# Performance work log

Hardware: AMD Instinct MI355X
Metric: run time of the kernel (lower is better)

The kernel has to match this reference:

```python
import jax, jax.numpy as jnp
import numpy as np

EPS = 1e-5
BS, NA, NC, NL, NPTS, ED, NG = 1, 900, 6, 4, 13, 256, 8
GD = ED // NG
IMG_W, IMG_H = 704.0, 256.0
FMAP_HW = [(64, 176), (32, 88), (16, 44), (8, 22)]


def _ln(x, g, b):
    m = x.mean(-1, keepdims=True)
    v = ((x - m) ** 2).mean(-1, keepdims=True)
    return (x - m) / jnp.sqrt(v + EPS) * g + b


def _grid_sample(img, grid):
    # img: [N,C,H,W]; grid: [N,P,Q,2] in [-1,1]; bilinear, zeros padding, align_corners=False
    N, C, H, W = img.shape
    gx = jnp.clip((grid[..., 0] + 1.0) * (W * 0.5) - 0.5, -1e4, 1e4)
    gy = jnp.clip((grid[..., 1] + 1.0) * (H * 0.5) - 0.5, -1e4, 1e4)
    x0 = jnp.floor(gx); y0 = jnp.floor(gy)
    wx1 = gx - x0; wy1 = gy - y0; wx0 = 1.0 - wx1; wy0 = 1.0 - wy1
    x0i = x0.astype(jnp.int32); y0i = y0.astype(jnp.int32)
    flat = img.reshape(N, C, H * W)

    def corner(xi, yi, wgt):
        valid = (xi >= 0) & (xi < W) & (yi >= 0) & (yi < H)
        idx = (jnp.clip(yi, 0, H - 1) * W + jnp.clip(xi, 0, W - 1))
        g = jax.vmap(lambda f, i: f[:, i])(flat, idx.reshape(N, -1))  # [N,C,P*Q]
        g = g.reshape(N, C, idx.shape[1], idx.shape[2])
        return g * (wgt * valid)[:, None]

    return (corner(x0i, y0i, wx0 * wy0) + corner(x0i + 1, y0i, wx1 * wy0)
            + corner(x0i, y0i + 1, wx0 * wy1) + corner(x0i + 1, y0i + 1, wx1 * wy1))


def setup_inputs() -> dict:
    key = jax.random.key(0)
    ks = jax.random.split(key, 20)
    d = {}
    d['instance_feature'] = jax.random.normal(ks[0], (BS, NA, ED), jnp.float32)
    xyz = jax.random.normal(ks[1], (BS, NA, 3), jnp.float32) * 1.5
    size = jax.random.normal(ks[2], (BS, NA, 3), jnp.float32) * 0.3
    theta = jax.random.uniform(ks[3], (BS, NA, 1), jnp.float32) * (2.0 * np.pi)
    vel = jax.random.normal(ks[4], (BS, NA, 3), jnp.float32) * 0.1
    d['anchor'] = jnp.concatenate([xyz, size, jnp.sin(theta), jnp.cos(theta), vel], -1)
    d['anchor_embed'] = jax.random.normal(ks[5], (BS, NA, ED), jnp.float32)
    for i, (h, w) in enumerate(FMAP_HW):
        d[f'fmap{i}'] = jax.random.normal(ks[6 + i], (BS, NC, ED, h, w), jnp.float32)
    base = jnp.array([[80., 0., 0., 352.], [0., 80., 0., 128.],
                      [0., 0., 0., 1.], [0., 0., 0., 1.]], jnp.float32)
    proj = jnp.tile(base, (BS, NC, 1, 1))
    proj = proj.at[:, :, :2, :].add(jax.random.normal(ks[10], (BS, NC, 2, 4), jnp.float32) * 2.0)
    d['projection_mat'] = proj
    d['image_wh'] = jnp.broadcast_to(jnp.array([IMG_W, IMG_H], jnp.float32), (BS, NC, 2))
    d['fix_scale'] = jnp.array([[0, 0, 0], [0.45, 0, 0], [-0.45, 0, 0], [0, 0.45, 0],
                                [0, -0.45, 0], [0, 0, 0.45], [0, 0, -0.45]], jnp.float32)

    def w(k, shape):
        return jax.random.normal(k, shape, jnp.float32) * 0.02

    d['lfc_w'] = w(ks[11], (ED, 6 * 3)); d['lfc_b'] = jnp.zeros((18,), jnp.float32)
    d['cam_w1'] = w(ks[12], (12, ED)); d['cam_b1'] = jnp.zeros((ED,), jnp.float32)
    d['cam_g1'] = jnp.ones((ED,), jnp.float32); d['cam_be1'] = jnp.zeros((ED,), jnp.float32)
    d['cam_w2'] = w(ks[13], (ED, ED)); d['cam_b2'] = jnp.zeros((ED,), jnp.float32)
    d['cam_g2'] = jnp.ones((ED,), jnp.float32); d['cam_be2'] = jnp.zeros((ED,), jnp.float32)
    d['wfc_w'] = w(ks[14], (ED, NG * NL * NPTS)); d['wfc_b'] = jnp.zeros((NG * NL * NPTS,), jnp.float32)
    d['op_w'] = w(ks[15], (ED, ED)); d['op_b'] = jnp.zeros((ED,), jnp.float32)
    return d


def reference(instance_feature, anchor, anchor_embed, fmap0, fmap1, fmap2, fmap3,
              projection_mat, image_wh, fix_scale, lfc_w, lfc_b,
              cam_w1, cam_b1, cam_g1, cam_be1, cam_w2, cam_b2, cam_g2, cam_be2,
              wfc_w, wfc_b, op_w, op_b):
    bs, na = instance_feature.shape[:2]
    # ---- keypoint generation ----
    size = jnp.exp(anchor[..., None, 3:6])                       # [bs,na,1,3]
    kp = fix_scale * size                                        # [bs,na,7,3]
    ls = jax.nn.sigmoid(instance_feature @ lfc_w + lfc_b).reshape(bs, na, -1, 3) - 0.5
    kp = jnp.concatenate([kp, ls * size], axis=-2)               # [bs,na,NPTS,3]
    sin, cos = anchor[..., 6:7], anchor[..., 7:8]                # [bs,na,1]
    kx, ky, kz = kp[..., 0], kp[..., 1], kp[..., 2]
    key_points = jnp.stack([cos * kx - sin * ky, sin * kx + cos * ky, kz], -1) \
                 + anchor[..., None, 0:3]                        # [bs,na,NPTS,3]
    # ---- per-cam/level/point group weights ----
    feat = instance_feature + anchor_embed
    cam_in = projection_mat[:, :, :3].reshape(bs, NC, 12)
    h = jax.nn.relu(cam_in @ cam_w1 + cam_b1); h = _ln(h, cam_g1, cam_be1)
    h = jax.nn.relu(h @ cam_w2 + cam_b2); cam_embed = _ln(h, cam_g2, cam_be2)
    f = feat[:, :, None] + cam_embed[:, None]                    # [bs,na,NC,ED]
    wts = (f @ wfc_w + wfc_b).reshape(bs, na, NC * NL * NPTS, NG)
    wts = jax.nn.softmax(wts, axis=-2).reshape(bs, na, NC, NL, NPTS, NG)
    # ---- multi-cam projection + bilinear sampling ----
    pts = jnp.concatenate([key_points, jnp.ones_like(key_points[..., :1])], -1)
    p2d = jnp.einsum('bcij,banj->bcani', projection_mat, pts)    # [bs,NC,na,NPTS,4]
    p2d = p2d[..., :2] / jnp.maximum(p2d[..., 2:3], 1e-5)
    p2d = p2d / image_wh[:, :, None, None]
    grid = (p2d * 2.0 - 1.0).reshape(bs * NC, na, NPTS, 2)
    feats = jnp.stack([_grid_sample(fm.reshape(bs * NC, ED, fm.shape[-2], fm.shape[-1]), grid)
                       for fm in (fmap0, fmap1, fmap2, fmap3)], axis=1)  # [bs*NC,NL,ED,na,NPTS]
    feats = feats.reshape(bs, NC, NL, ED, na, NPTS).transpose(0, 4, 1, 2, 5, 3)  # [bs,na,NC,NL,NPTS,ED]
    # ---- group-weighted fusion over cams & levels, then sum over points ----
    fg = feats.reshape(bs, na, NC, NL, NPTS, NG, GD)
    fused = jnp.einsum('bnclpg,bnclpgd->bnpgd', wts, fg).reshape(bs, na, NPTS, ED)
    fused = fused.sum(axis=2)                                    # [bs,na,ED]
    out = fused @ op_w + op_b
    return jnp.concatenate([out, instance_feature], axis=-1)     # [bs,na,2*ED]
```

## Files before the change

kernel.cpp:

```cpp
#include <hip/hip_runtime.h>
#include <stdint.h>

#define NA 900
#define NC 6
#define NL 4
#define NPTS 13
#define ED 256
#define NG 8
#define LNEPS 1e-5f
#define NSTAGE 718303
#define NSTAGE_BLOCKS 2806
#define NTRANS 1416
#define NCOPY 672
#define NSAMP 312
#define LGS 313

struct PIn { const void* p[24]; };

__device__ __forceinline__ float b2f(unsigned short u){
  union { uint32_t i; float f; } v; v.i = ((uint32_t)u)<<16; return v.f;
}
__device__ __forceinline__ unsigned short f2b(float f){
  union { float f; uint32_t i; } v; v.f = f;
  uint32_t r = v.i + 0x7FFFu + ((v.i>>16)&1u);
  return (unsigned short)(r>>16);
}
#define BLO(u) __uint_as_float((u)<<16)
#define BHI(u) __uint_as_float((u)&0xffff0000u)

__device__ __forceinline__ float ldx(const void* p, int i, bool bf){
  return bf ? b2f(((const unsigned short*)p)[i]) : ((const float*)p)[i];
}

__device__ __forceinline__ bool sniff_bf(const unsigned short* __restrict__ u16){
  int lane = threadIdx.x & 63;
  unsigned short u = u16[2*lane];
  int e = (u>>7)&0xFF;
  int sane = (e>=110 && e<=135) ? 1 : 0;
  #pragma unroll
  for (int m=32;m;m>>=1) sane += __shfl_xor(sane, m);
  return sane >= 48;
}

__device__ __forceinline__ void blockReduce2(float& a, float& b, float* lds){
  #pragma unroll
  for (int m=32;m;m>>=1){ a += __shfl_xor(a,m); b += __shfl_xor(b,m); }
  int w = threadIdx.x>>6;
  if ((threadIdx.x&63)==0){ lds[w]=a; lds[w+4]=b; }
  __syncthreads();
  a = lds[0]+lds[1]+lds[2]+lds[3];
  b = lds[4]+lds[5]+lds[6]+lds[7];
  __syncthreads();
}

__global__ __launch_bounds__(256) void k_prep(PIn in, float* __restrict__ stage,
                                              unsigned short* __restrict__ tf,
                                              unsigned short* __restrict__ wfcw_h,
                                              unsigned short* __restrict__ opw_h,
                                              float* __restrict__ Bc){
  const bool bf = sniff_bf((const unsigned short*)in.p[0]);
  const int tid = threadIdx.x;
  int b = blockIdx.x;

  __shared__ unsigned short TT[64][64];
  __shared__ float h[ED];
  __shared__ float cE[ED];
  __shared__ float red8[8];
  __shared__ float part[4][64];

  if (b < NSTAGE_BLOCKS){
    const int cum[21] = {0,230400,240300,470700,470796,470808,470829,475437,475455,
                         478527,478783,479039,479295,544831,545087,545343,545599,
                         652095,652511,718047,718303};
    const int map[20] = {0,1,2,7,8,9,10,11,12,13,14,15,16,17,18,19,20,21,22,23};
    int idx = b*256 + tid;
    if (idx >= NSTAGE) return;
    int seg = 0, base = 0;
    #pragma unroll
    for (int s=1;s<20;s++) if (idx >= cum[s]){ seg = s; base = cum[s]; }
    const void* src = in.p[map[0]];
    #pragma unroll
    for (int s=1;s<20;s++) if (seg==s) src = in.p[map[s]];
    stage[idx] = ldx(src, idx - base, bf);
    return;
  }
  b -= NSTAGE_BLOCKS;
  if (b < NTRANS){
    const int tiles[4] = {44,11,3,1};
    const int HWs[4]   = {11264,2816,704,176};
    const int TFO[4]   = {0,17301504,21626880,22708224};
    int l, local;
    if      (b < 1056){ l=0; local=b;      }
    else if (b < 1320){ l=1; local=b-1056; }
    else if (b < 1392){ l=2; local=b-1320; }
    else              { l=3; local=b-1392; }
    int pt = local % tiles[l]; int rest = local / tiles[l];
    int ct = rest & 3; int c = rest >> 2;
    const int HW = HWs[l];
    const int px0 = pt*256;
    const void* src = in.p[3+l];
    const int j8 = tid & 7;
    const int w8 = tid >> 3;

    uint4 v[2][4];
    if (bf){
      #pragma unroll
      for (int p=0;p<2;p++){
        int ch = ct*64 + p*32 + w8;
        size_t rowb = (size_t)(c*ED+ch)*HW;
        #pragma unroll
        for (int q=0;q<4;q++){
          int pxs = px0 + q*64 + j8*8;
          if (pxs < HW)
            v[p][q] = *reinterpret_cast<const uint4*>((const unsigned short*)src + rowb + pxs);
          else
            v[p][q] = make_uint4(0,0,0,0);
        }
      }
    }
    for (int q=0;q<4;q++){
      if (px0 + q*64 >= HW) break;
      if (!bf){
        #pragma unroll
        for (int p=0;p<2;p++){
          int ch = ct*64 + p*32 + w8;
          size_t rowb = (size_t)(c*ED+ch)*HW;
          int pxs = px0 + q*64 + j8*8;
          if (pxs < HW){
            float4 f0 = *reinterpret_cast<const float4*>((const float*)src + rowb + pxs);
            float4 f1 = *reinterpret_cast<const float4*>((const float*)src + rowb + pxs + 4);
            v[p][q].x = (uint32_t)f2b(f0.x) | ((uint32_t)f2b(f0.y)<<16);
            v[p][q].y = (uint32_t)f2b(f0.z) | ((uint32_t)f2b(f0.w)<<16);
            v[p][q].z = (uint32_t)f2b(f1.x) | ((uint32_t)f2b(f1.y)<<16);
            v[p][q].w = (uint32_t)f2b(f1.z) | ((uint32_t)f2b(f1.w)<<16);
          } else v[p][q] = make_uint4(0,0,0,0);
        }
      }
      #pragma unroll
      for (int p=0;p<2;p++){
        int r = p*32 + w8;
        int g8 = (j8 ^ (r>>3))<<3;
        *reinterpret_cast<uint4*>(&TT[r][g8]) = v[p][q];
      }
      __syncthreads();
      #pragma unroll
      for (int p=0;p<2;p++){
        int pxl = p*32 + w8;
        int px  = px0 + q*64 + pxl;
        int colq = (((pxl>>3) ^ j8)<<3) | (pxl & 7);
        int rb = j8*8;
        unsigned short t0 = TT[rb+0][colq], t1 = TT[rb+1][colq];
        unsigned short t2 = TT[rb+2][colq], t3 = TT[rb+3][colq];
        unsigned short t4 = TT[rb+4][colq], t5 = TT[rb+5][colq];
        unsigned short t6 = TT[rb+6][colq], t7 = TT[rb+7][colq];
        uint4 o;
        o.x = (uint32_t)t0 | ((uint32_t)t1<<16);
        o.y = (uint32_t)t2 | ((uint32_t)t3<<16);
        o.z = (uint32_t)t4 | ((uint32_t)t5<<16);
        o.w = (uint32_t)t6 | ((uint32_t)t7<<16);
        if (px < HW)
          *reinterpret_cast<uint4*>(tf + TFO[l] + (size_t)c*HW*ED + (size_t)px*ED + ct*64 + j8*8) = o;
      }
      __syncthreads();
    }
    return;
  }
  b -= NTRANS;
  if (b < NCOPY){
    int idx = b*256 + tid;
    if (idx < 106496){
      wfcw_h[idx] = bf ? ((const unsigned short*)in.p[20])[idx]
                       : f2b(((const float*)in.p[20])[idx]);
    } else {
      int j = idx - 106496;
      opw_h[j] = bf ? ((const unsigned short*)in.p[22])[j]
                    : f2b(((const float*)in.p[22])[j]);
    }
    return;
  }
  b -= NCOPY;
  {
    const void* proj = in.p[7];
    const void* w1 = in.p[12]; const void* b1 = in.p[13];
    const void* g1 = in.p[14]; const void* be1 = in.p[15];
    const void* w2 = in.p[16]; const void* b2 = in.p[17];
    const void* g2 = in.p[18]; const void* be2 = in.p[19];
    const void* wfcw = in.p[20]; const void* wfcb = in.p[21];
    const int c = b/7, colt = b - (b/7)*7;
    float ci[12];
    #pragma unroll
    for (int i=0;i<12;i++) ci[i] = ldx(proj, c*16+i, bf);
    float acc = ldx(b1, tid, bf);
    #pragma unroll
    for (int k=0;k<12;k++) acc += ci[k]*ldx(w1, k*ED+tid, bf);
    float x = fmaxf(acc, 0.f);
    float s=x, q=x*x;
    blockReduce2(s,q,red8);
    float mean = s*(1.f/ED), var = q*(1.f/ED)-mean*mean;
    h[tid] = (x-mean)*rsqrtf(var+LNEPS)*ldx(g1,tid,bf) + ldx(be1,tid,bf);
    __syncthreads();
    acc = ldx(b2, tid, bf);
    #pragma unroll 8
    for (int k=0;k<ED;k++) acc += h[k]*ldx(w2, k*ED+tid, bf);
    x = fmaxf(acc,0.f);
    s=x; q=x*x;
    blockReduce2(s,q,red8);
    mean = s*(1.f/ED); var = q*(1.f/ED)-mean*mean;
    cE[tid] = (x-mean)*rsqrtf(var+LNEPS)*ldx(g2,tid,bf) + ldx(be2,tid,bf);
    __syncthreads();
    const int kc = tid>>6, colL = tid&63, col = colt*64+colL;
    float a = 0.f;
    if (col < 416){
      #pragma unroll 8
      for (int k=0;k<64;k++) a += cE[kc*64+k]*ldx(wfcw, (kc*64+k)*416+col, bf);
    }
    part[kc][colL] = a;
    __syncthreads();
    if (kc==0 && col<416)
      Bc[c*416+col] = part[0][colL]+part[1][colL]+part[2][colL]+part[3][colL] + ldx(wfcb,col,bf);
  }
}

__global__ __launch_bounds__(512, 4) void k_anchor(
    const float* __restrict__ stage, const unsigned short* __restrict__ tf,
    const unsigned short* __restrict__ wfcw_h, const unsigned short* __restrict__ opw_h,
    const float* __restrict__ Bc, const void* __restrict__ rawinst,
    void* __restrict__ outv){
  const int n = blockIdx.x, tid = threadIdx.x;
  const bool bf = sniff_bf((const unsigned short*)rawinst);

  const float* s_inst = stage + 0;
  const float* s_anc  = stage + 230400;
  const float* s_ae   = stage + 240300;
  const float* s_proj = stage + 470700;
  const float* s_imwh = stage + 470796;
  const float* s_fixs = stage + 470808;
  const float* s_lw   = stage + 470829;
  const float* s_lb   = stage + 475437;
  const float* s_opb  = stage + 718047;

  __shared__ float ifs[ED];
  __shared__ float fe[ED];
  __shared__ float lg2[8*LGS];
  __shared__ uint4 cbi[NSAMP];
  __shared__ uint4 cwf[NSAMP];
  __shared__ unsigned short coff[NSAMP];
  __shared__ float red[16][ED+4];
  __shared__ float fu[ED];
  __shared__ float kp[13][3];
  __shared__ float sc[8];
  __shared__ float lsv[18];
  __shared__ int scnt;

  if (tid < 256){
    float iv = s_inst[n*ED+tid];
    ifs[tid] = iv;
    fe[tid]  = iv + s_ae[n*ED+tid];
  } else {
    int t = tid - 256;
    if (t == 0)      scnt = 0;
    if (t < 3)       sc[t] = s_anc[n*11+t];
    else if (t == 3) sc[3] = s_anc[n*11+6];
    else if (t == 4) sc[4] = s_anc[n*11+7];
    else if (t < 8)  sc[t] = __expf(s_anc[n*11+t-2]);
  }
  __syncthreads();
  if (tid < 144){
    int d = tid>>3, j = tid&7;
    float a = 0.f;
    #pragma unroll 8
    for (int k=j*32;k<j*32+32;k++) a += ifs[k]*s_lw[k*18+d];
    a += __shfl_xor(a,1); a += __shfl_xor(a,2); a += __shfl_xor(a,4);
    if (j==0){
      a += s_lb[d];
      lsv[d] = 1.f/(1.f+__expf(-a)) - 0.5f;
    }
  }
  __syncthreads();
  if (tid < 13){
    float kx,ky,kz;
    if (tid < 7){
      kx = s_fixs[tid*3+0]*sc[5];
      ky = s_fixs[tid*3+1]*sc[6];
      kz = s_fixs[tid*3+2]*sc[7];
    } else {
      int j = tid-7;
      kx = lsv[j*3+0]*sc[5]; ky = lsv[j*3+1]*sc[6]; kz = lsv[j*3+2]*sc[7];
    }
    kp[tid][0] = sc[4]*kx - sc[3]*ky + sc[0];
    kp[tid][1] = sc[3]*kx + sc[4]*ky + sc[1];
    kp[tid][2] = kz + sc[2];
  }
  if (tid < 416){
    float a0 = 0.f;
    #pragma unroll 8
    for (int k=0;k<ED;k++) a0 += fe[k]*b2f(wfcw_h[k*416+tid]);
    const int g = tid & 7, rr = tid >> 3;
    #pragma unroll
    for (int c=0;c<NC;c++)
      lg2[g*LGS + c*52 + rr] = a0 + Bc[c*416+tid];
  }
  __syncthreads();
  if (tid < NSAMP){
    int s = tid;
    int c = s/52, rr = s - c*52;
    int l = rr/13, p = rr - l*13;
    float m[12];
    #pragma unroll
    for (int i=0;i<12;i++) m[i] = s_proj[c*16+i];
    float X=kp[p][0], Y=kp[p][1], Z=kp[p][2];
    float x = m[0]*X + m[1]*Y + m[2]*Z  + m[3];
    float y = m[4]*X + m[5]*Y + m[6]*Z  + m[7];
    float z = m[8]*X + m[9]*Y + m[10]*Z + m[11];
    float d = fmaxf(z, 1e-5f);
    float px = x/(d*s_imwh[c*2+0]), py = y/(d*s_imwh[c*2+1]);
    const int W = 176>>l, H = 64>>l;
    const int TFO[4] = {0,17301504,21626880,22708224};
    float gx = fminf(fmaxf(px*(float)W - 0.5f, -10000.f), 10000.f);
    float gy = fminf(fmaxf(py*(float)H - 0.5f, -10000.f), 10000.f);
    float xf = floorf(gx), yf = floorf(gy);
    int x0 = (int)xf, y0 = (int)yf;
    float wx1 = gx-xf, wy1 = gy-yf;
    float wx0 = 1.f-wx1, wy0 = 1.f-wy1;
    bool vx0 = (x0>=0)&&(x0<W),   vx1 = (x0+1>=0)&&(x0+1<W);
    bool vy0 = (y0>=0)&&(y0<H),   vy1 = (y0+1>=0)&&(y0+1<H);
    float w00 = (vx0&&vy0) ? wx0*wy0 : 0.f;
    float w10 = (vx1&&vy0) ? wx1*wy0 : 0.f;
    float w01 = (vx0&&vy1) ? wx0*wy1 : 0.f;
    float w11 = (vx1&&vy1) ? wx1*wy1 : 0.f;
    if (w00+w10+w01+w11 != 0.f){
      int cx0 = min(max(x0,0),W-1), cx1 = min(max(x0+1,0),W-1);
      int cy0 = min(max(y0,0),H-1), cy1 = min(max(y0+1,0),H-1);
      uint32_t cam = (uint32_t)TFO[l] + (uint32_t)(c*H*W)*ED;
      uint4 bi, wv;
      bi.x = cam + (uint32_t)(cy0*W+cx0)*ED;
      bi.y = cam + (uint32_t)(cy0*W+cx1)*ED;
      bi.z = cam + (uint32_t)(cy1*W+cx0)*ED;
      bi.w = cam + (uint32_t)(cy1*W+cx1)*ED;
      wv.x = __float_as_uint(w00); wv.y = __float_as_uint(w10);
      wv.z = __float_as_uint(w01); wv.w = __float_as_uint(w11);
      int slot = atomicAdd(&scnt, 1);
      cbi[slot] = bi;
      cwf[slot] = wv;
      coff[slot] = (unsigned short)s;
    }
  }
  {
    const int g = tid>>6, j = tid&63;
    float v[5]; float mx = -1e30f;
    #pragma unroll
    for (int i=0;i<5;i++){
      int e = j + 64*i;
      float val = -1e30f;
      if (e < NSAMP){
        val = lg2[g*LGS + e];
        mx = fmaxf(mx, val);
      }
      v[i] = val;
    }
    #pragma unroll
    for (int mk=32;mk;mk>>=1) mx = fmaxf(mx, __shfl_xor(mx, mk));
    float sum = 0.f;
    #pragma unroll
    for (int i=0;i<5;i++){
      if (j + 64*i < NSAMP){ float ex = __expf(v[i]-mx); v[i] = ex; sum += ex; }
    }
    #pragma unroll
    for (int mk=32;mk;mk>>=1) sum += __shfl_xor(sum, mk);
    float inv = 1.f/sum;
    #pragma unroll
    for (int i=0;i<5;i++){
      int e = j + 64*i;
      if (e < NSAMP) lg2[g*LGS + e] = v[i]*inv;
    }
  }
  __syncthreads();
  {
    const int m = scnt;
    const int strm = tid>>5, lane32 = tid&31;
    const int ch8 = lane32*8, gg = lane32>>2;
    float acc[8] = {0,0,0,0,0,0,0,0};
    int i = strm;
    for (; i + 16 < m; i += 32){
      uint4 biA = cbi[i],    wfA = cwf[i];
      uint4 biB = cbi[i+16], wfB = cwf[i+16];
      float wgA = lg2[gg*LGS + coff[i]],  wgB = lg2[gg*LGS + coff[i+16]];
      uint4 a00 = *reinterpret_cast<const uint4*>(tf + biA.x + ch8);
      uint4 a10 = *reinterpret_cast<const uint4*>(tf + biA.y + ch8);
      uint4 a01 = *reinterpret_cast<const uint4*>(tf + biA.z + ch8);
      uint4 a11 = *reinterpret_cast<const uint4*>(tf + biA.w + ch8);
      uint4 b00 = *reinterpret_cast<const uint4*>(tf + biB.x + ch8);
      uint4 b10 = *reinterpret_cast<const uint4*>(tf + biB.y + ch8);
      uint4 b01 = *reinterpret_cast<const uint4*>(tf + biB.z + ch8);
      uint4 b11 = *reinterpret_cast<const uint4*>(tf + biB.w + ch8);
      float pA00 = wgA*__uint_as_float(wfA.x), pA10 = wgA*__uint_as_float(wfA.y);
      float pA01 = wgA*__uint_as_float(wfA.z), pA11 = wgA*__uint_as_float(wfA.w);
      float pB00 = wgB*__uint_as_float(wfB.x), pB10 = wgB*__uint_as_float(wfB.y);
      float pB01 = wgB*__uint_as_float(wfB.z), pB11 = wgB*__uint_as_float(wfB.w);
      acc[0] += pA00*BLO(a00.x)+pA10*BLO(a10.x)+pA01*BLO(a01.x)+pA11*BLO(a11.x)
              + pB00*BLO(b00.x)+pB10*BLO(b10.x)+pB01*BLO(b01.x)+pB11*BLO(b11.x);
      acc[1] += pA00*BHI(a00.x)+pA10*BHI(a10.x)+pA01*BHI(a01.x)+pA11*BHI(a11.x)
              + pB00*BHI(b00.x)+pB10*BHI(b10.x)+pB01*BHI(b01.x)+pB11*BHI(b11.x);
      acc[2] += pA00*BLO(a00.y)+pA10*BLO(a10.y)+pA01*BLO(a01.y)+pA11*BLO(a11.y)
              + pB00*BLO(b00.y)+pB10*BLO(b10.y)+pB01*BLO(b01.y)+pB11*BLO(b11.y);
      acc[3] += pA00*BHI(a00.y)+pA10*BHI(a10.y)+pA01*BHI(a01.y)+pA11*BHI(a11.y)
              + pB00*BHI(b00.y)+pB10*BHI(b10.y)+pB01*BHI(b01.y)+pB11*BHI(b11.y);
      acc[4] += pA00*BLO(a00.z)+pA10*BLO(a10.z)+pA01*BLO(a01.z)+pA11*BLO(a11.z)
              + pB00*BLO(b00.z)+pB10*BLO(b10.z)+pB01*BLO(b01.z)+pB11*BLO(b11.z);
      acc[5] += pA00*BHI(a00.z)+pA10*BHI(a10.z)+pA01*BHI(a01.z)+pA11*BHI(a11.z)
              + pB00*BHI(b00.z)+pB10*BHI(b10.z)+pB01*BHI(b01.z)+pB11*BHI(b11.z);
      acc[6] += pA00*BLO(a00.w)+pA10*BLO(a10.w)+pA01*BLO(a01.w)+pA11*BLO(a11.w)
              + pB00*BLO(b00.w)+pB10*BLO(b10.w)+pB01*BLO(b01.w)+pB11*BLO(b11.w);
      acc[7] += pA00*BHI(a00.w)+pA10*BHI(a10.w)+pA01*BHI(a01.w)+pA11*BHI(a11.w)
              + pB00*BHI(b00.w)+pB10*BHI(b10.w)+pB01*BHI(b01.w)+pB11*BHI(b11.w);
    }
    for (; i < m; i += 16){
      uint4 bi = cbi[i], wf = cwf[i];
      float wg = lg2[gg*LGS + coff[i]];
      uint4 q00 = *reinterpret_cast<const uint4*>(tf + bi.x + ch8);
      uint4 q10 = *reinterpret_cast<const uint4*>(tf + bi.y + ch8);
      uint4 q01 = *reinterpret_cast<const uint4*>(tf + bi.z + ch8);
      uint4 q11 = *reinterpret_cast<const uint4*>(tf + bi.w + ch8);
      float p00 = wg*__uint_as_float(wf.x), p10 = wg*__uint_as_float(wf.y);
      float p01 = wg*__uint_as_float(wf.z), p11 = wg*__uint_as_float(wf.w);
      acc[0] += p00*BLO(q00.x)+p10*BLO(q10.x)+p01*BLO(q01.x)+p11*BLO(q11.x);
      acc[1] += p00*BHI(q00.x)+p10*BHI(q10.x)+p01*BHI(q01.x)+p11*BHI(q11.x);
      acc[2] += p00*BLO(q00.y)+p10*BLO(q10.y)+p01*BLO(q01.y)+p11*BLO(q11.y);
      acc[3] += p00*BHI(q00.y)+p10*BHI(q10.y)+p01*BHI(q01.y)+p11*BHI(q11.y);
      acc[4] += p00*BLO(q00.z)+p10*BLO(q10.z)+p01*BLO(q01.z)+p11*BLO(q11.z);
      acc[5] += p00*BHI(q00.z)+p10*BHI(q10.z)+p01*BHI(q01.z)+p11*BHI(q11.z);
      acc[6] += p00*BLO(q00.w)+p10*BLO(q10.w)+p01*BLO(q01.w)+p11*BLO(q11.w);
      acc[7] += p00*BHI(q00.w)+p10*BHI(q10.w)+p01*BHI(q01.w)+p11*BHI(q11.w);
    }
    *reinterpret_cast<float4*>(&red[strm][ch8])   = make_float4(acc[0],acc[1],acc[2],acc[3]);
    *reinterpret_cast<float4*>(&red[strm][ch8+4]) = make_float4(acc[4],acc[5],acc[6],acc[7]);
  }
  __syncthreads();
  if (tid < 256){
    float r = 0.f;
    #pragma unroll
    for (int i=0;i<16;i++) r += red[i][tid];
    fu[tid] = r;
  }
  __syncthreads();
  {
    const int col = tid & 255, half = tid >> 8;
    const int k0 = half*128;
    float a = 0.f;
    #pragma unroll 8
    for (int k=k0;k<k0+128;k++) a += fu[k]*b2f(opw_h[k*ED+col]);
    red[half][col] = a;
  }
  __syncthreads();
  {
    float v;
    if (tid < 256) v = s_opb[tid] + red[0][tid] + red[1][tid];
    else           v = ifs[tid-256];
    if (bf) ((unsigned short*)outv)[n*512+tid] = f2b(v);
    else    ((float*)outv)[n*512+tid]          = v;
  }
}

extern "C" void kernel_launch(void* const* d_in, const int* in_sizes, int n_in,
                              void* d_out, int out_size, void* d_ws, size_t ws_size,
                              hipStream_t stream){
  char* ws = (char*)d_ws;
  size_t off = 0;
  auto alloc = [&](size_t bytes)->char*{
    char* p = ws + off; off += (bytes + 63) & ~size_t(63); return p;
  };
  unsigned short* tf = (unsigned short*)alloc((size_t)22978560*2);
  float* stage  = (float*)alloc((size_t)NSTAGE*4);
  unsigned short* wfcw_h = (unsigned short*)alloc((size_t)106496*2);
  unsigned short* opw_h  = (unsigned short*)alloc((size_t)65536*2);
  float* Bc     = (float*)alloc((size_t)NC*416*4);

  PIn in;
  for (int i=0;i<24;i++) in.p[i] = d_in[i];

  k_prep<<<NSTAGE_BLOCKS + NTRANS + NCOPY + 42, 256, 0, stream>>>(in, stage, tf, wfcw_h, opw_h, Bc);
  k_anchor<<<NA, 512, 0, stream>>>(stage, tf, wfcw_h, opw_h, Bc, d_in[0], d_out);
}
```

Baseline: 253.9 us.

## Split anchor kernel into descriptor, split-gather and output-projection kernels

The single per-anchor kernel is replaced by three kernels. One builds the sampling descriptors, with softmax weights baked in, into global memory. One runs the bilinear gather with 4 blocks per anchor for more parallelism and occupancy. One reduces the partials and applies the output projection. This spreads the memory-bound gather over more blocks, at the cost of two extra launches and global round-trips for the descriptors and partial sums.

```diff
diff --git a/kernel.cpp b/kernel.cpp
--- a/kernel.cpp
+++ b/kernel.cpp
@@ -14,6 +14,8 @@
 #define NCOPY 672
 #define NSAMP 312
 #define LGS 313
+#define SPLITS 4
+#define CHMAX 78
 
 struct PIn { const void* p[24]; };
 
@@ -221,11 +223,10 @@
   }
 }
 
-__global__ __launch_bounds__(512, 4) void k_anchor(
-    const float* __restrict__ stage, const unsigned short* __restrict__ tf,
-    const unsigned short* __restrict__ wfcw_h, const unsigned short* __restrict__ opw_h,
+__global__ __launch_bounds__(256) void k_desc(
+    const float* __restrict__ stage, const unsigned short* __restrict__ wfcw_h,
     const float* __restrict__ Bc, const void* __restrict__ rawinst,
-    void* __restrict__ outv){
+    uint4* __restrict__ gdesc, int* __restrict__ mcnt, void* __restrict__ outv){
   const int n = blockIdx.x, tid = threadIdx.x;
   const bool bf = sniff_bf((const unsigned short*)rawinst);
 
@@ -237,32 +238,29 @@
   const float* s_fixs = stage + 470808;
   const float* s_lw   = stage + 470829;
   const float* s_lb   = stage + 475437;
-  const float* s_opb  = stage + 718047;
 
   __shared__ float ifs[ED];
   __shared__ float fe[ED];
   __shared__ float lg2[8*LGS];
-  __shared__ uint4 cbi[NSAMP];
-  __shared__ uint4 cwf[NSAMP];
-  __shared__ unsigned short coff[NSAMP];
-  __shared__ float red[16][ED+4];
-  __shared__ float fu[ED];
   __shared__ float kp[13][3];
   __shared__ float sc[8];
   __shared__ float lsv[18];
   __shared__ int scnt;
 
-  if (tid < 256){
+  {
+    if (tid==0) scnt = 0;
     float iv = s_inst[n*ED+tid];
     ifs[tid] = iv;
     fe[tid]  = iv + s_ae[n*ED+tid];
-  } else {
-    int t = tid - 256;
-    if (t == 0)      scnt = 0;
-    if (t < 3)       sc[t] = s_anc[n*11+t];
-    else if (t == 3) sc[3] = s_anc[n*11+6];
-    else if (t == 4) sc[4] = s_anc[n*11+7];
-    else if (t < 8)  sc[t] = __expf(s_anc[n*11+t-2]);
+    if (bf) ((unsigned short*)outv)[n*512+256+tid] = f2b(iv);
+    else    ((float*)outv)[n*512+256+tid]          = iv;
+    if (tid >= 256-8){
+      int t = tid - (256-8);
+      if (t < 3)       sc[t] = s_anc[n*11+t];
+      else if (t == 3) sc[3] = s_anc[n*11+6];
+      else if (t == 4) sc[4] = s_anc[n*11+7];
+      else             sc[t] = __expf(s_anc[n*11+t-2]);
+    }
   }
   __syncthreads();
   if (tid < 144){
@@ -291,174 +289,214 @@
     kp[tid][1] = sc[3]*kx + sc[4]*ky + sc[1];
     kp[tid][2] = kz + sc[2];
   }
-  if (tid < 416){
-    float a0 = 0.f;
-    #pragma unroll 8
-    for (int k=0;k<ED;k++) a0 += fe[k]*b2f(wfcw_h[k*416+tid]);
+  {
+    int col2 = (tid < 160) ? tid+256 : 415;
+    float a0 = 0.f, a1 = 0.f;
+    #pragma unroll 4
+    for (int k=0;k<ED;k++){
+      float fv = fe[k];
+      a0 += fv*b2f(wfcw_h[k*416+tid]);
+      a1 += fv*b2f(wfcw_h[k*416+col2]);
+    }
     const int g = tid & 7, rr = tid >> 3;
-    #pragma unroll
-    for (int c=0;c<NC;c++)
+    const int g2 = col2 & 7, rr2 = col2 >> 3;
+    #pragma unroll
+    for (int c=0;c<NC;c++){
       lg2[g*LGS + c*52 + rr] = a0 + Bc[c*416+tid];
-  }
-  __syncthreads();
-  if (tid < NSAMP){
-    int s = tid;
-    int c = s/52, rr = s - c*52;
-    int l = rr/13, p = rr - l*13;
-    float m[12];
-    #pragma unroll
-    for (int i=0;i<12;i++) m[i] = s_proj[c*16+i];
-    float X=kp[p][0], Y=kp[p][1], Z=kp[p][2];
-    float x = m[0]*X + m[1]*Y + m[2]*Z  + m[3];
-    float y = m[4]*X + m[5]*Y + m[6]*Z  + m[7];
-    float z = m[8]*X + m[9]*Y + m[10]*Z + m[11];
-    float d = fmaxf(z, 1e-5f);
-    float px = x/(d*s_imwh[c*2+0]), py = y/(d*s_imwh[c*2+1]);
-    const int W = 176>>l, H = 64>>l;
-    const int TFO[4] = {0,17301504,21626880,22708224};
-    float gx = fminf(fmaxf(px*(float)W - 0.5f, -10000.f), 10000.f);
-    float gy = fminf(fmaxf(py*(float)H - 0.5f, -10000.f), 10000.f);
-    float xf = floorf(gx), yf = floorf(gy);
-    int x0 = (int)xf, y0 = (int)yf;
-    float wx1 = gx-xf, wy1 = gy-yf;
-    float wx0 = 1.f-wx1, wy0 = 1.f-wy1;
-    bool vx0 = (x0>=0)&&(x0<W),   vx1 = (x0+1>=0)&&(x0+1<W);
-    bool vy0 = (y0>=0)&&(y0<H),   vy1 = (y0+1>=0)&&(y0+1<H);
-    float w00 = (vx0&&vy0) ? wx0*wy0 : 0.f;
-    float w10 = (vx1&&vy0) ? wx1*wy0 : 0.f;
-    float w01 = (vx0&&vy1) ? wx0*wy1 : 0.f;
-    float w11 = (vx1&&vy1) ? wx1*wy1 : 0.f;
-    if (w00+w10+w01+w11 != 0.f){
-      int cx0 = min(max(x0,0),W-1), cx1 = min(max(x0+1,0),W-1);
-      int cy0 = min(max(y0,0),H-1), cy1 = min(max(y0+1,0),H-1);
-      uint32_t cam = (uint32_t)TFO[l] + (uint32_t)(c*H*W)*ED;
-      uint4 bi, wv;
-      bi.x = cam + (uint32_t)(cy0*W+cx0)*ED;
-      bi.y = cam + (uint32_t)(cy0*W+cx1)*ED;
-      bi.z = cam + (uint32_t)(cy1*W+cx0)*ED;
-      bi.w = cam + (uint32_t)(cy1*W+cx1)*ED;
-      wv.x = __float_as_uint(w00); wv.y = __float_as_uint(w10);
-      wv.z = __float_as_uint(w01); wv.w = __float_as_uint(w11);
-      int slot = atomicAdd(&scnt, 1);
-      cbi[slot] = bi;
-      cwf[slot] = wv;
-      coff[slot] = (unsigned short)s;
-    }
-  }
+      if (tid < 160) lg2[g2*LGS + c*52 + rr2] = a1 + Bc[c*416+col2];
+    }
+  }
+  __syncthreads();
   {
-    const int g = tid>>6, j = tid&63;
-    float v[5]; float mx = -1e30f;
-    #pragma unroll
-    for (int i=0;i<5;i++){
-      int e = j + 64*i;
+    const int g = tid>>5, j = tid&31;
+    float v[10]; float mx = -1e30f;
+    #pragma unroll
+    for (int i=0;i<10;i++){
+      int e = j + 32*i;
       float val = -1e30f;
-      if (e < NSAMP){
-        val = lg2[g*LGS + e];
-        mx = fmaxf(mx, val);
+      if (e < NSAMP){ val = lg2[g*LGS + e]; mx = fmaxf(mx, val); }
+      v[i] = val;
+    }
+    #pragma unroll
+    for (int mk=16;mk;mk>>=1) mx = fmaxf(mx, __shfl_xor(mx, mk, 32));
+    float sum = 0.f;
+    #pragma unroll
+    for (int i=0;i<10;i++){
+      if (j + 32*i < NSAMP){ float ex = __expf(v[i]-mx); v[i] = ex; sum += ex; }
+    }
+    #pragma unroll
+    for (int mk=16;mk;mk>>=1) sum += __shfl_xor(sum, mk, 32);
+    float inv = 1.f/sum;
+    #pragma unroll
+    for (int i=0;i<10;i++){
+      int e = j + 32*i;
+      if (e < NSAMP) lg2[g*LGS + e] = v[i]*inv;
+    }
+  }
+  __syncthreads();
+  #pragma unroll
+  for (int pass=0;pass<2;pass++){
+    int s = tid + pass*256;
+    if (s < NSAMP){
+      int c = s/52, rr = s - c*52;
+      int l = rr/13, p = rr - l*13;
+      float m[12];
+      #pragma unroll
+      for (int i=0;i<12;i++) m[i] = s_proj[c*16+i];
+      float X=kp[p][0], Y=kp[p][1], Z=kp[p][2];
+      float x = m[0]*X + m[1]*Y + m[2]*Z  + m[3];
+      float y = m[4]*X + m[5]*Y + m[6]*Z  + m[7];
+      float z = m[8]*X + m[9]*Y + m[10]*Z + m[11];
+      float d = fmaxf(z, 1e-5f);
+      float px = x/(d*s_imwh[c*2+0]), py = y/(d*s_imwh[c*2+1]);
+      const int W = 176>>l, H = 64>>l;
+      const int TFO[4] = {0,17301504,21626880,22708224};
+      float gx = fminf(fmaxf(px*(float)W - 0.5f, -10000.f), 10000.f);
+      float gy = fminf(fmaxf(py*(float)H - 0.5f, -10000.f), 10000.f);
+      float xf = floorf(gx), yf = floorf(gy);
+      int x0 = (int)xf, y0 = (int)yf;
+      float wx1 = gx-xf, wy1 = gy-yf;
+      float wx0 = 1.f-wx1, wy0 = 1.f-wy1;
+      bool vx0 = (x0>=0)&&(x0<W),   vx1 = (x0+1>=0)&&(x0+1<W);
+      bool vy0 = (y0>=0)&&(y0<H),   vy1 = (y0+1>=0)&&(y0+1<H);
+      float w00 = (vx0&&vy0) ? wx0*wy0 : 0.f;
+      float w10 = (vx1&&vy0) ? wx1*wy0 : 0.f;
+      float w01 = (vx0&&vy1) ? wx0*wy1 : 0.f;
+      float w11 = (vx1&&vy1) ? wx1*wy1 : 0.f;
+      if (w00+w10+w01+w11 != 0.f){
+        int cx0 = min(max(x0,0),W-1), cx1 = min(max(x0+1,0),W-1);
+        int cy0 = min(max(y0,0),H-1), cy1 = min(max(y0+1,0),H-1);
+        uint32_t cam = (uint32_t)TFO[l] + (uint32_t)(c*H*W)*ED;
+        uint4 bi, wv;
+        bi.x = cam + (uint32_t)(cy0*W+cx0)*ED;
+        bi.y = cam + (uint32_t)(cy0*W+cx1)*ED;
+        bi.z = cam + (uint32_t)(cy1*W+cx0)*ED;
+        bi.w = cam + (uint32_t)(cy1*W+cx1)*ED;
+        wv.x = __float_as_uint(w00); wv.y = __float_as_uint(w10);
+        wv.z = __float_as_uint(w01); wv.w = __float_as_uint(w11);
+        float4 wa = make_float4(lg2[0*LGS+s], lg2[1*LGS+s], lg2[2*LGS+s], lg2[3*LGS+s]);
+        float4 wb = make_float4(lg2[4*LGS+s], lg2[5*LGS+s], lg2[6*LGS+s], lg2[7*LGS+s]);
+        int slot = atomicAdd(&scnt, 1);
+        uint4* dst = gdesc + (size_t)(n*NSAMP + slot)*4;
+        dst[0] = bi;
+        dst[1] = wv;
+        dst[2] = *reinterpret_cast<uint4*>(&wa);
+        dst[3] = *reinterpret_cast<uint4*>(&wb);
       }
-      v[i] = val;
-    }
-    #pragma unroll
-    for (int mk=32;mk;mk>>=1) mx = fmaxf(mx, __shfl_xor(mx, mk));
-    float sum = 0.f;
-    #pragma unroll
-    for (int i=0;i<5;i++){
-      if (j + 64*i < NSAMP){ float ex = __expf(v[i]-mx); v[i] = ex; sum += ex; }
-    }
-    #pragma unroll
-    for (int mk=32;mk;mk>>=1) sum += __shfl_xor(sum, mk);
-    float inv = 1.f/sum;
-    #pragma unroll
-    for (int i=0;i<5;i++){
-      int e = j + 64*i;
-      if (e < NSAMP) lg2[g*LGS + e] = v[i]*inv;
-    }
-  }
-  __syncthreads();
+    }
+  }
+  __syncthreads();
+  if (tid==0) mcnt[n] = scnt;
+}
+
+__global__ __launch_bounds__(256, 6) void k_gather(
+    const unsigned short* __restrict__ tf, const uint4* __restrict__ gdesc,
+    const int* __restrict__ mcnt, float* __restrict__ partial){
+  const int bid = blockIdx.x;
+  const int n = bid >> 2, sp = bid & 3;
+  const int tid = threadIdx.x;
+  const int m = mcnt[n];
+  const int chunk = (m + SPLITS-1) >> 2;
+  const int i0 = sp*chunk;
+  int cnt = m - i0; if (cnt > chunk) cnt = chunk; if (cnt < 0) cnt = 0;
+
+  __shared__ uint4 ldesc[CHMAX*4];
+  __shared__ float red[4][ED+4];
+
   {
-    const int m = scnt;
-    const int strm = tid>>5, lane32 = tid&31;
-    const int ch8 = lane32*8, gg = lane32>>2;
-    float acc[8] = {0,0,0,0,0,0,0,0};
-    int i = strm;
-    for (; i + 16 < m; i += 32){
-      uint4 biA = cbi[i],    wfA = cwf[i];
-      uint4 biB = cbi[i+16], wfB = cwf[i+16];
-      float wgA = lg2[gg*LGS + coff[i]],  wgB = lg2[gg*LGS + coff[i+16]];
-      uint4 a00 = *reinterpret_cast<const uint4*>(tf + biA.x + ch8);
-      uint4 a10 = *reinterpret_cast<const uint4*>(tf + biA.y + ch8);
-      uint4 a01 = *reinterpret_cast<const uint4*>(tf + biA.z + ch8);
-      uint4 a11 = *reinterpret_cast<const uint4*>(tf + biA.w + ch8);
-      uint4 b00 = *reinterpret_cast<const uint4*>(tf + biB.x + ch8);
-      uint4 b10 = *reinterpret_cast<const uint4*>(tf + biB.y + ch8);
-      uint4 b01 = *reinterpret_cast<const uint4*>(tf + biB.z + ch8);
-      uint4 b11 = *reinterpret_cast<const uint4*>(tf + biB.w + ch8);
-      float pA00 = wgA*__uint_as_float(wfA.x), pA10 = wgA*__uint_as_float(wfA.y);
-      float pA01 = wgA*__uint_as_float(wfA.z), pA11 = wgA*__uint_as_float(wfA.w);
-      float pB00 = wgB*__uint_as_float(wfB.x), pB10 = wgB*__uint_as_float(wfB.y);
-      float pB01 = wgB*__uint_as_float(wfB.z), pB11 = wgB*__uint_as_float(wfB.w);
-      acc[0] += pA00*BLO(a00.x)+pA10*BLO(a10.x)+pA01*BLO(a01.x)+pA11*BLO(a11.x)
-              + pB00*BLO(b00.x)+pB10*BLO(b10.x)+pB01*BLO(b01.x)+pB11*BLO(b11.x);
-      acc[1] += pA00*BHI(a00.x)+pA10*BHI(a10.x)+pA01*BHI(a01.x)+pA11*BHI(a11.x)
-              + pB00*BHI(b00.x)+pB10*BHI(b10.x)+pB01*BHI(b01.x)+pB11*BHI(b11.x);
-      acc[2] += pA00*BLO(a00.y)+pA10*BLO(a10.y)+pA01*BLO(a01.y)+pA11*BLO(a11.y)
-              + pB00*BLO(b00.y)+pB10*BLO(b10.y)+pB01*BLO(b01.y)+pB11*BLO(b11.y);
-      acc[3] += pA00*BHI(a00.y)+pA10*BHI(a10.y)+pA01*BHI(a01.y)+pA11*BHI(a11.y)
-              + pB00*BHI(b00.y)+pB10*BHI(b10.y)+pB01*BHI(b01.y)+pB11*BHI(b11.y);
-      acc[4] += pA00*BLO(a00.z)+pA10*BLO(a10.z)+pA01*BLO(a01.z)+pA11*BLO(a11.z)
-              + pB00*BLO(b00.z)+pB10*BLO(b10.z)+pB01*BLO(b01.z)+pB11*BLO(b11.z);
-      acc[5] += pA00*BHI(a00.z)+pA10*BHI(a10.z)+pA01*BHI(a01.z)+pA11*BHI(a11.z)
-              + pB00*BHI(b00.z)+pB10*BHI(b10.z)+pB01*BHI(b01.z)+pB11*BHI(b11.z);
-      acc[6] += pA00*BLO(a00.w)+pA10*BLO(a10.w)+pA01*BLO(a01.w)+pA11*BLO(a11.w)
-              + pB00*BLO(b00.w)+pB10*BLO(b10.w)+pB01*BLO(b01.w)+pB11*BLO(b11.w);
-      acc[7] += pA00*BHI(a00.w)+pA10*BHI(a10.w)+pA01*BHI(a01.w)+pA11*BHI(a11.w)
-              + pB00*BHI(b00.w)+pB10*BHI(b10.w)+pB01*BHI(b01.w)+pB11*BHI(b11.w);
-    }
-    for (; i < m; i += 16){
-      uint4 bi = cbi[i], wf = cwf[i];
-      float wg = lg2[gg*LGS + coff[i]];
-      uint4 q00 = *reinterpret_cast<const uint4*>(tf + bi.x + ch8);
-      uint4 q10 = *reinterpret_cast<const uint4*>(tf + bi.y + ch8);
-      uint4 q01 = *reinterpret_cast<const uint4*>(tf + bi.z + ch8);
-      uint4 q11 = *reinterpret_cast<const uint4*>(tf + bi.w + ch8);
-      float p00 = wg*__uint_as_float(wf.x), p10 = wg*__uint_as_float(wf.y);
-      float p01 = wg*__uint_as_float(wf.z), p11 = wg*__uint_as_float(wf.w);
-      acc[0] += p00*BLO(q00.x)+p10*BLO(q10.x)+p01*BLO(q01.x)+p11*BLO(q11.x);
-      acc[1] += p00*BHI(q00.x)+p10*BHI(q10.x)+p01*BHI(q01.x)+p11*BHI(q11.x);
-      acc[2] += p00*BLO(q00.y)+p10*BLO(q10.y)+p01*BLO(q01.y)+p11*BLO(q11.y);
-      acc[3] += p00*BHI(q00.y)+p10*BHI(q10.y)+p01*BHI(q01.y)+p11*BHI(q11.y);
-      acc[4] += p00*BLO(q00.z)+p10*BLO(q10.z)+p01*BLO(q01.z)+p11*BLO(q11.z);
-      acc[5] += p00*BHI(q00.z)+p10*BHI(q10.z)+p01*BHI(q01.z)+p11*BHI(q11.z);
-      acc[6] += p00*BLO(q00.w)+p10*BLO(q10.w)+p01*BLO(q01.w)+p11*BLO(q11.w);
-      acc[7] += p00*BHI(q00.w)+p10*BHI(q10.w)+p01*BHI(q01.w)+p11*BHI(q11.w);
-    }
-    *reinterpret_cast<float4*>(&red[strm][ch8])   = make_float4(acc[0],acc[1],acc[2],acc[3]);
-    *reinterpret_cast<float4*>(&red[strm][ch8+4]) = make_float4(acc[4],acc[5],acc[6],acc[7]);
-  }
-  __syncthreads();
-  if (tid < 256){
+    const uint4* src = gdesc + (size_t)(n*NSAMP + i0)*4;
+    for (int j=tid; j < cnt*4; j += 256) ldesc[j] = src[j];
+  }
+  __syncthreads();
+
+  const int strm = tid>>5, lane32 = tid&31;
+  const int ch8 = lane32*8, gg = lane32>>2;
+  float acc[8] = {0,0,0,0,0,0,0,0};
+  int i = strm;
+  for (; i + 8 < cnt; i += 16){
+    uint4 biA = ldesc[i*4],     wfA = ldesc[i*4+1];
+    uint4 biB = ldesc[(i+8)*4], wfB = ldesc[(i+8)*4+1];
+    float wgA = reinterpret_cast<const float*>(&ldesc[i*4+2])[gg];
+    float wgB = reinterpret_cast<const float*>(&ldesc[(i+8)*4+2])[gg];
+    uint4 a00 = *reinterpret_cast<const uint4*>(tf + biA.x + ch8);
+    uint4 a10 = *reinterpret_cast<const uint4*>(tf + biA.y + ch8);
+    uint4 a01 = *reinterpret_cast<const uint4*>(tf + biA.z + ch8);
+    uint4 a11 = *reinterpret_cast<const uint4*>(tf + biA.w + ch8);
+    uint4 b00 = *reinterpret_cast<const uint4*>(tf + biB.x + ch8);
+    uint4 b10 = *reinterpret_cast<const uint4*>(tf + biB.y + ch8);
+    uint4 b01 = *reinterpret_cast<const uint4*>(tf + biB.z + ch8);
+    uint4 b11 = *reinterpret_cast<const uint4*>(tf + biB.w + ch8);
+    float pA00 = wgA*__uint_as_float(wfA.x), pA10 = wgA*__uint_as_float(wfA.y);
+    float pA01 = wgA*__uint_as_float(wfA.z), pA11 = wgA*__uint_as_float(wfA.w);
+    float pB00 = wgB*__uint_as_float(wfB.x), pB10 = wgB*__uint_as_float(wfB.y);
+    float pB01 = wgB*__uint_as_float(wfB.z), pB11 = wgB*__uint_as_float(wfB.w);
+    acc[0] += pA00*BLO(a00.x)+pA10*BLO(a10.x)+pA01*BLO(a01.x)+pA11*BLO(a11.x)
+            + pB00*BLO(b00.x)+pB10*BLO(b10.x)+pB01*BLO(b01.x)+pB11*BLO(b11.x);
+    acc[1] += pA00*BHI(a00.x)+pA10*BHI(a10.x)+pA01*BHI(a01.x)+pA11*BHI(a11.x)
+            + pB00*BHI(b00.x)+pB10*BHI(b10.x)+pB01*BHI(b01.x)+pB11*BHI(b11.x);
+    acc[2] += pA00*BLO(a00.y)+pA10*BLO(a10.y)+pA01*BLO(a01.y)+pA11*BLO(a11.y)
+            + pB00*BLO(b00.y)+pB10*BLO(b10.y)+pB01*BLO(b01.y)+pB11*BLO(b11.y);
+    acc[3] += pA00*BHI(a00.y)+pA10*BHI(a10.y)+pA01*BHI(a01.y)+pA11*BHI(a11.y)
+            + pB00*BHI(b00.y)+pB10*BHI(b10.y)+pB01*BHI(b01.y)+pB11*BHI(b11.y);
+    acc[4] += pA00*BLO(a00.z)+pA10*BLO(a10.z)+pA01*BLO(a01.z)+pA11*BLO(a11.z)
+            + pB00*BLO(b00.z)+pB10*BLO(b10.z)+pB01*BLO(b01.z)+pB11*BLO(b11.z);
+    acc[5] += pA00*BHI(a00.z)+pA10*BHI(a10.z)+pA01*BHI(a01.z)+pA11*BHI(a11.z)
+            + pB00*BHI(b00.z)+pB10*BHI(b10.z)+pB01*BHI(b01.z)+pB11*BHI(b11.z);
+    acc[6] += pA00*BLO(a00.w)+pA10*BLO(a10.w)+pA01*BLO(a01.w)+pA11*BLO(a11.w)
+            + pB00*BLO(b00.w)+pB10*BLO(b10.w)+pB01*BLO(b01.w)+pB11*BLO(b11.w);
+    acc[7] += pA00*BHI(a00.w)+pA10*BHI(a10.w)+pA01*BHI(a01.w)+pA11*BHI(a11.w)
+            + pB00*BHI(b00.w)+pB10*BHI(b10.w)+pB01*BHI(b01.w)+pB11*BHI(b11.w);
+  }
+  for (; i < cnt; i += 8){
+    uint4 bi = ldesc[i*4], wf = ldesc[i*4+1];
+    float wg = reinterpret_cast<const float*>(&ldesc[i*4+2])[gg];
+    uint4 q00 = *reinterpret_cast<const uint4*>(tf + bi.x + ch8);
+    uint4 q10 = *reinterpret_cast<const uint4*>(tf + bi.y + ch8);
+    uint4 q01 = *reinterpret_cast<const uint4*>(tf + bi.z + ch8);
+    uint4 q11 = *reinterpret_cast<const uint4*>(tf + bi.w + ch8);
+    float p00 = wg*__uint_as_float(wf.x), p10 = wg*__uint_as_float(wf.y);
+    float p01 = wg*__uint_as_float(wf.z), p11 = wg*__uint_as_float(wf.w);
+    acc[0] += p00*BLO(q00.x)+p10*BLO(q10.x)+p01*BLO(q01.x)+p11*BLO(q11.x);
+    acc[1] += p00*BHI(q00.x)+p10*BHI(q10.x)+p01*BHI(q01.x)+p11*BHI(q11.x);
+    acc[2] += p00*BLO(q00.y)+p10*BLO(q10.y)+p01*BLO(q01.y)+p11*BLO(q11.y);
+    acc[3] += p00*BHI(q00.y)+p10*BHI(q10.y)+p01*BHI(q01.y)+p11*BHI(q11.y);
+    acc[4] += p00*BLO(q00.z)+p10*BLO(q10.z)+p01*BLO(q01.z)+p11*BLO(q11.z);
+    acc[5] += p00*BHI(q00.z)+p10*BHI(q10.z)+p01*BHI(q01.z)+p11*BHI(q11.z);
+    acc[6] += p00*BLO(q00.w)+p10*BLO(q10.w)+p01*BLO(q01.w)+p11*BLO(q11.w);
+    acc[7] += p00*BHI(q00.w)+p10*BHI(q10.w)+p01*BHI(q01.w)+p11*BHI(q11.w);
+  }
+  #pragma unroll
+  for (int j=0;j<8;j++) acc[j] += __shfl_xor(acc[j], 32);
+  const int w = tid>>6;
+  if ((tid&63) < 32){
+    *reinterpret_cast<float4*>(&red[w][ch8])   = make_float4(acc[0],acc[1],acc[2],acc[3]);
+    *reinterpret_cast<float4*>(&red[w][ch8+4]) = make_float4(acc[4],acc[5],acc[6],acc[7]);
+  }
+  __syncthreads();
+  float r = red[0][tid] + red[1][tid] + red[2][tid] + red[3][tid];
+  partial[(size_t)(sp*NA + n)*ED + tid] = r;
+}
+
+__global__ __launch_bounds__(256) void k_out(
+    const float* __restrict__ stage, const unsigned short* __restrict__ opw_h,
+    const float* __restrict__ partial, const void* __restrict__ rawinst,
+    void* __restrict__ outv){
+  const int n = blockIdx.x, tid = threadIdx.x;
+  const bool bf = sniff_bf((const unsigned short*)rawinst);
+  const float* s_opb = stage + 718047;
+  __shared__ float fu[ED];
+  {
     float r = 0.f;
     #pragma unroll
-    for (int i=0;i<16;i++) r += red[i][tid];
+    for (int sp=0;sp<SPLITS;sp++) r += partial[(size_t)(sp*NA + n)*ED + tid];
     fu[tid] = r;
   }
   __syncthreads();
-  {
-    const int col = tid & 255, half = tid >> 8;
-    const int k0 = half*128;
-    float a = 0.f;
-    #pragma unroll 8
-    for (int k=k0;k<k0+128;k++) a += fu[k]*b2f(opw_h[k*ED+col]);
-    red[half][col] = a;
-  }
-  __syncthreads();
-  {
-    float v;
-    if (tid < 256) v = s_opb[tid] + red[0][tid] + red[1][tid];
-    else           v = ifs[tid-256];
-    if (bf) ((unsigned short*)outv)[n*512+tid] = f2b(v);
-    else    ((float*)outv)[n*512+tid]          = v;
-  }
+  float acc = s_opb[tid];
+  #pragma unroll 4
+  for (int k=0;k<ED;k++) acc += fu[k]*b2f(opw_h[k*ED+tid]);
+  if (bf) ((unsigned short*)outv)[n*512+tid] = f2b(acc);
+  else    ((float*)outv)[n*512+tid]          = acc;
 }
 
 extern "C" void kernel_launch(void* const* d_in, const int* in_sizes, int n_in,
@@ -474,10 +512,15 @@
   unsigned short* wfcw_h = (unsigned short*)alloc((size_t)106496*2);
   unsigned short* opw_h  = (unsigned short*)alloc((size_t)65536*2);
   float* Bc     = (float*)alloc((size_t)NC*416*4);
+  uint4* gdesc  = (uint4*)alloc((size_t)NA*NSAMP*64);
+  int*   mcnt   = (int*)alloc((size_t)NA*4);
+  float* partial= (float*)alloc((size_t)SPLITS*NA*ED*4);
 
   PIn in;
   for (int i=0;i<24;i++) in.p[i] = d_in[i];
 
   k_prep<<<NSTAGE_BLOCKS + NTRANS + NCOPY + 42, 256, 0, stream>>>(in, stage, tf, wfcw_h, opw_h, Bc);
-  k_anchor<<<NA, 512, 0, stream>>>(stage, tf, wfcw_h, opw_h, Bc, d_in[0], d_out);
-}
+  k_desc<<<NA, 256, 0, stream>>>(stage, wfcw_h, Bc, d_in[0], gdesc, mcnt, d_out);
+  k_gather<<<NA*SPLITS, 256, 0, stream>>>(tf, gdesc, mcnt, partial);
+  k_out<<<NA, 256, 0, stream>>>(stage, opw_h, partial, d_in[0], d_out);
+}
```

After: 270.2 us. 6.4% more time.
